# Kernel optimization log

Hardware: AMD Instinct MI355X
Metric: run time of the kernel (lower is better)

Reference implementation:

```python
import jax, jax.numpy as jnp
import numpy as np

N_NODES = 100000
D_SRC = 128
D_DST = 128
D_OUT = 256
N_EDGES = 600000


def setup_inputs() -> dict:
    key = jax.random.key(0)
    k1, k2, k3, k4, k5 = jax.random.split(key, 5)
    x_src = jax.random.normal(k1, (N_NODES, D_SRC), dtype=jnp.float32)
    x_dst = jax.random.normal(k2, (N_NODES, D_DST), dtype=jnp.float32)
    edge_index = jax.random.randint(k3, (2, N_EDGES), 0, N_NODES, dtype=jnp.int64)
    # Linear(in_src + in_dst, out): torch stores W as [out, in]
    fan_in = D_SRC + D_DST
    bound = 1.0 / np.sqrt(fan_in)
    W = jax.random.uniform(k4, (D_OUT, fan_in), minval=-bound, maxval=bound, dtype=jnp.float32)
    b = jax.random.uniform(k5, (D_OUT,), minval=-bound, maxval=bound, dtype=jnp.float32)
    return {"x_src": x_src, "x_dst": x_dst, "edge_index": edge_index, "W": W, "b": b}


def reference(x_src, x_dst, edge_index, W, b):
    src_idx, dst_idx = edge_index[0], edge_index[1]
    n_dst = x_dst.shape[0]
    x_j = x_src[src_idx]                                  # [E, D_SRC] gather
    summed = jax.ops.segment_sum(x_j, dst_idx, num_segments=n_dst)   # [N, D_SRC]
    count = jax.ops.segment_sum(jnp.ones((src_idx.shape[0],), dtype=x_src.dtype),
                                dst_idx, num_segments=n_dst)          # [N]
    agg = summed / jnp.maximum(count, 1.0)[:, None]        # scatter-mean
    h = jnp.concatenate([x_dst, agg], axis=-1)             # [N, D_DST+D_SRC]
    return jax.nn.relu(h @ W.T + b)                        # [N, D_OUT]
```

## Files before the change

kernel.cpp:

```cpp
#include <hip/hip_runtime.h>

#define N_NODES 100000
#define D_SRC 128
#define D_OUT 256
#define K_DIM 256
#define CAP 32
#define OVF_CAP 2048

typedef __attribute__((ext_vector_type(8))) short short8;
typedef __attribute__((ext_vector_type(4))) float float4v;

__device__ inline unsigned short f2bf(float f) {
    unsigned int u = __float_as_uint(f);
    u += 0x7FFF + ((u >> 16) & 1);
    return (unsigned short)(u >> 16);
}

__global__ __launch_bounds__(256) void bucket_kernel(
    const int* __restrict__ ei,
    int* __restrict__ deg,
    int* __restrict__ ovf_cnt,
    int* __restrict__ ovf,
    int* __restrict__ bucket,
    int n_edges)
{
    int e = blockIdx.x * 256 + threadIdx.x;
    if (e >= n_edges) return;
    int s = ei[e];
    int d = ei[n_edges + e];
    int pos = atomicAdd(deg + d, 1);
    if (pos < CAP) {
        bucket[(size_t)d * CAP + pos] = s;
    } else {
        int o = atomicAdd(ovf_cnt, 1);
        if (o < OVF_CAP) { ovf[2 * o] = s; ovf[2 * o + 1] = d; }
    }
}

__global__ __launch_bounds__(256) void gather_kernel(
    const float* __restrict__ x_src,
    const int*   __restrict__ deg,
    const int*   __restrict__ bucket,
    float*       __restrict__ agg)
{
    int node = blockIdx.x * 4 + (threadIdx.x >> 6);
    if (node >= N_NODES) return;
    int lane = threadIdx.x & 63;

    int n = deg[node];
    n = (n < CAP) ? n : CAP;

    int idx = bucket[(size_t)node * CAP + (lane & 31)];

    float2 acc0 = make_float2(0.f, 0.f);
    float2 acc1 = make_float2(0.f, 0.f);
    int i = 0;
    for (; i + 2 <= n; i += 2) {
        int s0 = __shfl(idx, i);
        int s1 = __shfl(idx, i + 1);
        float2 v0 = *(const float2*)(x_src + (size_t)s0 * D_SRC + lane * 2);
        float2 v1 = *(const float2*)(x_src + (size_t)s1 * D_SRC + lane * 2);
        acc0.x += v0.x; acc0.y += v0.y;
        acc1.x += v1.x; acc1.y += v1.y;
    }
    if (i < n) {
        int s0 = __shfl(idx, i);
        float2 v0 = *(const float2*)(x_src + (size_t)s0 * D_SRC + lane * 2);
        acc0.x += v0.x; acc0.y += v0.y;
    }
    acc0.x += acc1.x; acc0.y += acc1.y;
    *(float2*)(agg + (size_t)node * D_SRC + lane * 2) = acc0;
}

__global__ __launch_bounds__(256) void ovf_fixup_kernel(
    const float* __restrict__ x_src,
    const int* __restrict__ ovf_cnt,
    const int* __restrict__ ovf,
    float* __restrict__ agg)
{
    int e = blockIdx.x * 8 + (threadIdx.x >> 5);
    int lane = threadIdx.x & 31;
    int n = *ovf_cnt;
    if (n > OVF_CAP) n = OVF_CAP;
    if (e >= n) return;
    int s = ovf[2 * e];
    int d = ovf[2 * e + 1];
    float4 v = ((const float4*)(x_src + (size_t)s * D_SRC))[lane];
    float* a = agg + (size_t)d * D_SRC + lane * 4;
    unsafeAtomicAdd(a + 0, v.x);
    unsafeAtomicAdd(a + 1, v.y);
    unsafeAtomicAdd(a + 2, v.z);
    unsafeAtomicAdd(a + 3, v.w);
}

__global__ __launch_bounds__(256) void convert_w_kernel(
    const float* __restrict__ W, unsigned short* __restrict__ Wb)
{
    int i = blockIdx.x * 256 + threadIdx.x;
    float4 v = ((const float4*)W)[i];
    ushort4 o;
    o.x = f2bf(v.x); o.y = f2bf(v.y); o.z = f2bf(v.z); o.w = f2bf(v.w);
    ((ushort4*)Wb)[i] = o;
}

#define BM 128
#define BK 32
#define PADK 40

__global__ __launch_bounds__(512) void mfma_gemm_kernel(
    const float* __restrict__ x_dst,
    const float* __restrict__ agg,
    const int*   __restrict__ deg,
    const unsigned short* __restrict__ Wb,
    const float* __restrict__ bias,
    float*       __restrict__ out)
{
    __shared__ unsigned short As[BM * PADK];
    __shared__ unsigned short Bs[D_OUT * PADK];
    __shared__ float inv_s[BM];

    int t = threadIdx.x;
    int m0 = blockIdx.x * BM;

    if (t < BM) {
        int m = m0 + t;
        int c = (m < N_NODES) ? deg[m] : 1;
        inv_s[t] = 1.0f / (float)((c > 1) ? c : 1);
    }
    __syncthreads();

    int wave = t >> 6;
    int lane = t & 63;
    int wm = wave >> 2;
    int wn = wave & 3;
    int lrow = lane & 15;
    int kq = lane >> 4;

    float4v acc[4][4];
    #pragma unroll
    for (int i = 0; i < 4; ++i)
        #pragma unroll
        for (int j = 0; j < 4; ++j)
            acc[i][j] = (float4v){0.f, 0.f, 0.f, 0.f};

    int a_row  = t >> 2;
    int a_kseg = (t & 3) * 8;

    for (int kc = 0; kc < K_DIM / BK; ++kc) {
        int k0 = kc * BK;

        {
            bool is_agg = (k0 >= 128);
            const float* src = is_agg ? agg : x_dst;
            int koff = (is_agg ? k0 - 128 : k0) + a_kseg;
            int grow = m0 + a_row;
            float4 v0 = make_float4(0.f, 0.f, 0.f, 0.f);
            float4 v1 = v0;
            if (grow < N_NODES) {
                const float* p = src + (size_t)grow * D_SRC + koff;
                v0 = *(const float4*)p;
                v1 = *(const float4*)(p + 4);
            }
            if (is_agg) {
                float iv = inv_s[a_row];
                v0.x *= iv; v0.y *= iv; v0.z *= iv; v0.w *= iv;
                v1.x *= iv; v1.y *= iv; v1.z *= iv; v1.w *= iv;
            }
            union { unsigned short s[8]; short8 v; } pk;
            pk.s[0] = f2bf(v0.x); pk.s[1] = f2bf(v0.y);
            pk.s[2] = f2bf(v0.z); pk.s[3] = f2bf(v0.w);
            pk.s[4] = f2bf(v1.x); pk.s[5] = f2bf(v1.y);
            pk.s[6] = f2bf(v1.z); pk.s[7] = f2bf(v1.w);
            *(short8*)&As[a_row * PADK + a_kseg] = pk.v;
        }

        #pragma unroll
        for (int r = 0; r < 2; ++r) {
            int i = r * 512 + t;
            int row  = i >> 2;
            int kseg = (i & 3) * 8;
            short8 w = *(const short8*)(Wb + (size_t)row * K_DIM + k0 + kseg);
            *(short8*)&Bs[row * PADK + kseg] = w;
        }
        __syncthreads();

        short8 afrag[4], bfrag[4];
        #pragma unroll
        for (int mf = 0; mf < 4; ++mf)
            afrag[mf] = *(short8*)&As[(wm * 64 + mf * 16 + lrow) * PADK + kq * 8];
        #pragma unroll
        for (int nf = 0; nf < 4; ++nf)
            bfrag[nf] = *(short8*)&Bs[(wn * 64 + nf * 16 + lrow) * PADK + kq * 8];
        #pragma unroll
        for (int mf = 0; mf < 4; ++mf)
            #pragma unroll
            for (int nf = 0; nf < 4; ++nf)
                acc[mf][nf] = __builtin_amdgcn_mfma_f32_16x16x32_bf16(
                    afrag[mf], bfrag[nf], acc[mf][nf], 0, 0, 0);
        __syncthreads();
    }

    #pragma unroll
    for (int nf = 0; nf < 4; ++nf) {
        int col = wn * 64 + nf * 16 + lrow;
        float bv = bias[col];
        #pragma unroll
        for (int mf = 0; mf < 4; ++mf) {
            int rbase = m0 + wm * 64 + mf * 16 + kq * 4;
            #pragma unroll
            for (int r = 0; r < 4; ++r) {
                int row = rbase + r;
                if (row < N_NODES)
                    out[(size_t)row * D_OUT + col] = fmaxf(acc[mf][nf][r] + bv, 0.f);
            }
        }
    }
}

extern "C" void kernel_launch(void* const* d_in, const int* in_sizes, int n_in,
                              void* d_out, int out_size, void* d_ws, size_t ws_size,
                              hipStream_t stream) {
    const float* x_src = (const float*)d_in[0];
    const float* x_dst = (const float*)d_in[1];
    const int*   ei    = (const int*)d_in[2];
    const float* W     = (const float*)d_in[3];
    const float* bias  = (const float*)d_in[4];
    float* out = (float*)d_out;

    int n_edges = in_sizes[2] / 2;

    int* deg     = (int*)d_ws;
    int* ovf_cnt = deg + N_NODES;
    int* ovf     = ovf_cnt + 4;
    int* bucket  = ovf + OVF_CAP * 2;
    float* agg   = (float*)(bucket + (size_t)N_NODES * CAP);
    unsigned short* Wb = (unsigned short*)(agg + (size_t)N_NODES * D_SRC);

    hipMemsetAsync(d_ws, 0, (N_NODES + 4) * sizeof(int), stream);

    bucket_kernel<<<(n_edges + 255) / 256, 256, 0, stream>>>(
        ei, deg, ovf_cnt, ovf, bucket, n_edges);

    convert_w_kernel<<<(D_OUT * K_DIM / 4 + 255) / 256, 256, 0, stream>>>(W, Wb);

    gather_kernel<<<(N_NODES + 3) / 4, 256, 0, stream>>>(
        x_src, deg, bucket, agg);

    ovf_fixup_kernel<<<OVF_CAP / 8, 256, 0, stream>>>(
        x_src, ovf_cnt, ovf, agg);

    mfma_gemm_kernel<<<(N_NODES + BM - 1) / BM, 512, 0, stream>>>(
        x_dst, agg, deg, Wb, bias, out);
}
```

Before: 344.0 us.

## Fold overflow fixup and mean scaling into gather, store bf16 agg, drop LDS in GEMM

The gather kernel now handles overflow edges itself with a linear scan of the overflow list for high-degree nodes. It also applies the mean division and writes the aggregate as bf16, which halves agg traffic and removes the separate fixup launch. The GEMM drops shared-memory staging and barriers: each wave loads A and B fragments straight from global memory in MFMA layout, with 64-row blocks of 256 threads. The cost is redundant global reads of W and A across waves, which now rely on the cache. High-degree nodes also pay a serial scan of the overflow list.

```diff
diff --git a/kernel.cpp b/kernel.cpp
--- a/kernel.cpp
+++ b/kernel.cpp
@@ -41,14 +41,16 @@
     const float* __restrict__ x_src,
     const int*   __restrict__ deg,
     const int*   __restrict__ bucket,
-    float*       __restrict__ agg)
+    const int*   __restrict__ ovf_cnt,
+    const int*   __restrict__ ovf,
+    unsigned short* __restrict__ aggb)
 {
     int node = blockIdx.x * 4 + (threadIdx.x >> 6);
     if (node >= N_NODES) return;
     int lane = threadIdx.x & 63;
 
-    int n = deg[node];
-    n = (n < CAP) ? n : CAP;
+    int dtot = deg[node];
+    int n = (dtot < CAP) ? dtot : CAP;
 
     int idx = bucket[(size_t)node * CAP + (lane & 31)];
 
@@ -69,28 +71,23 @@
         acc0.x += v0.x; acc0.y += v0.y;
     }
     acc0.x += acc1.x; acc0.y += acc1.y;
-    *(float2*)(agg + (size_t)node * D_SRC + lane * 2) = acc0;
-}
-
-__global__ __launch_bounds__(256) void ovf_fixup_kernel(
-    const float* __restrict__ x_src,
-    const int* __restrict__ ovf_cnt,
-    const int* __restrict__ ovf,
-    float* __restrict__ agg)
-{
-    int e = blockIdx.x * 8 + (threadIdx.x >> 5);
-    int lane = threadIdx.x & 31;
-    int n = *ovf_cnt;
-    if (n > OVF_CAP) n = OVF_CAP;
-    if (e >= n) return;
-    int s = ovf[2 * e];
-    int d = ovf[2 * e + 1];
-    float4 v = ((const float4*)(x_src + (size_t)s * D_SRC))[lane];
-    float* a = agg + (size_t)d * D_SRC + lane * 4;
-    unsafeAtomicAdd(a + 0, v.x);
-    unsafeAtomicAdd(a + 1, v.y);
-    unsafeAtomicAdd(a + 2, v.z);
-    unsafeAtomicAdd(a + 3, v.w);
+
+    if (dtot > CAP) {
+        int oc = *ovf_cnt;
+        if (oc > OVF_CAP) oc = OVF_CAP;
+        for (int o = 0; o < oc; ++o) {
+            if (ovf[2 * o + 1] == node) {
+                int s0 = ovf[2 * o];
+                float2 v0 = *(const float2*)(x_src + (size_t)s0 * D_SRC + lane * 2);
+                acc0.x += v0.x; acc0.y += v0.y;
+            }
+        }
+    }
+
+    float inv = 1.0f / (float)((dtot > 1) ? dtot : 1);
+    unsigned int packed = (unsigned int)f2bf(acc0.x * inv)
+                        | ((unsigned int)f2bf(acc0.y * inv) << 16);
+    ((unsigned int*)(aggb + (size_t)node * D_SRC))[lane] = packed;
 }
 
 __global__ __launch_bounds__(256) void convert_w_kernel(
@@ -103,38 +100,19 @@
     ((ushort4*)Wb)[i] = o;
 }
 
-#define BM 128
-#define BK 32
-#define PADK 40
-
-__global__ __launch_bounds__(512) void mfma_gemm_kernel(
+__global__ __launch_bounds__(256) void mfma_gemm_kernel(
     const float* __restrict__ x_dst,
-    const float* __restrict__ agg,
-    const int*   __restrict__ deg,
+    const unsigned short* __restrict__ aggb,
     const unsigned short* __restrict__ Wb,
     const float* __restrict__ bias,
     float*       __restrict__ out)
 {
-    __shared__ unsigned short As[BM * PADK];
-    __shared__ unsigned short Bs[D_OUT * PADK];
-    __shared__ float inv_s[BM];
-
-    int t = threadIdx.x;
-    int m0 = blockIdx.x * BM;
-
-    if (t < BM) {
-        int m = m0 + t;
-        int c = (m < N_NODES) ? deg[m] : 1;
-        inv_s[t] = 1.0f / (float)((c > 1) ? c : 1);
-    }
-    __syncthreads();
-
-    int wave = t >> 6;
-    int lane = t & 63;
-    int wm = wave >> 2;
-    int wn = wave & 3;
+    int wave = threadIdx.x >> 6;
+    int lane = threadIdx.x & 63;
     int lrow = lane & 15;
-    int kq = lane >> 4;
+    int kq   = lane >> 4;
+    int m0 = blockIdx.x * 64;
+    int n0 = wave * 64;
 
     float4v acc[4][4];
     #pragma unroll
@@ -143,70 +121,65 @@
         for (int j = 0; j < 4; ++j)
             acc[i][j] = (float4v){0.f, 0.f, 0.f, 0.f};
 
-    int a_row  = t >> 2;
-    int a_kseg = (t & 3) * 8;
-
-    for (int kc = 0; kc < K_DIM / BK; ++kc) {
-        int k0 = kc * BK;
-
-        {
-            bool is_agg = (k0 >= 128);
-            const float* src = is_agg ? agg : x_dst;
-            int koff = (is_agg ? k0 - 128 : k0) + a_kseg;
-            int grow = m0 + a_row;
-            float4 v0 = make_float4(0.f, 0.f, 0.f, 0.f);
-            float4 v1 = v0;
-            if (grow < N_NODES) {
-                const float* p = src + (size_t)grow * D_SRC + koff;
-                v0 = *(const float4*)p;
-                v1 = *(const float4*)(p + 4);
+    int  rowv[4];
+    bool rok[4];
+    #pragma unroll
+    for (int mf = 0; mf < 4; ++mf) {
+        rowv[mf] = m0 + mf * 16 + lrow;
+        rok[mf]  = rowv[mf] < N_NODES;
+    }
+
+    const short8 zfrag = (short8){0,0,0,0,0,0,0,0};
+
+    #pragma unroll
+    for (int kc = 0; kc < 8; ++kc) {
+        const int k0 = kc * 32;
+        short8 afrag[4], bfrag[4];
+
+        if (kc < 4) {
+            #pragma unroll
+            for (int mf = 0; mf < 4; ++mf) {
+                float4 v0 = make_float4(0.f, 0.f, 0.f, 0.f);
+                float4 v1 = v0;
+                if (rok[mf]) {
+                    const float* p = x_dst + (size_t)rowv[mf] * D_SRC + k0 + kq * 8;
+                    v0 = *(const float4*)p;
+                    v1 = *(const float4*)(p + 4);
+                }
+                union { unsigned short s[8]; short8 v; } pk;
+                pk.s[0] = f2bf(v0.x); pk.s[1] = f2bf(v0.y);
+                pk.s[2] = f2bf(v0.z); pk.s[3] = f2bf(v0.w);
+                pk.s[4] = f2bf(v1.x); pk.s[5] = f2bf(v1.y);
+                pk.s[6] = f2bf(v1.z); pk.s[7] = f2bf(v1.w);
+                afrag[mf] = pk.v;
             }
-            if (is_agg) {
-                float iv = inv_s[a_row];
-                v0.x *= iv; v0.y *= iv; v0.z *= iv; v0.w *= iv;
-                v1.x *= iv; v1.y *= iv; v1.z *= iv; v1.w *= iv;
-            }
-            union { unsigned short s[8]; short8 v; } pk;
-            pk.s[0] = f2bf(v0.x); pk.s[1] = f2bf(v0.y);
-            pk.s[2] = f2bf(v0.z); pk.s[3] = f2bf(v0.w);
-            pk.s[4] = f2bf(v1.x); pk.s[5] = f2bf(v1.y);
-            pk.s[6] = f2bf(v1.z); pk.s[7] = f2bf(v1.w);
-            *(short8*)&As[a_row * PADK + a_kseg] = pk.v;
+        } else {
+            #pragma unroll
+            for (int mf = 0; mf < 4; ++mf)
+                afrag[mf] = rok[mf]
+                    ? *(const short8*)(aggb + (size_t)rowv[mf] * D_SRC + (k0 - 128) + kq * 8)
+                    : zfrag;
         }
 
         #pragma unroll
-        for (int r = 0; r < 2; ++r) {
-            int i = r * 512 + t;
-            int row  = i >> 2;
-            int kseg = (i & 3) * 8;
-            short8 w = *(const short8*)(Wb + (size_t)row * K_DIM + k0 + kseg);
-            *(short8*)&Bs[row * PADK + kseg] = w;
-        }
-        __syncthreads();
-
-        short8 afrag[4], bfrag[4];
-        #pragma unroll
-        for (int mf = 0; mf < 4; ++mf)
-            afrag[mf] = *(short8*)&As[(wm * 64 + mf * 16 + lrow) * PADK + kq * 8];
-        #pragma unroll
         for (int nf = 0; nf < 4; ++nf)
-            bfrag[nf] = *(short8*)&Bs[(wn * 64 + nf * 16 + lrow) * PADK + kq * 8];
+            bfrag[nf] = *(const short8*)(Wb + (size_t)(n0 + nf * 16 + lrow) * K_DIM + k0 + kq * 8);
+
         #pragma unroll
         for (int mf = 0; mf < 4; ++mf)
             #pragma unroll
             for (int nf = 0; nf < 4; ++nf)
                 acc[mf][nf] = __builtin_amdgcn_mfma_f32_16x16x32_bf16(
                     afrag[mf], bfrag[nf], acc[mf][nf], 0, 0, 0);
-        __syncthreads();
     }
 
     #pragma unroll
     for (int nf = 0; nf < 4; ++nf) {
-        int col = wn * 64 + nf * 16 + lrow;
+        int col = n0 + nf * 16 + lrow;
         float bv = bias[col];
         #pragma unroll
         for (int mf = 0; mf < 4; ++mf) {
-            int rbase = m0 + wm * 64 + mf * 16 + kq * 4;
+            int rbase = m0 + mf * 16 + kq * 4;
             #pragma unroll
             for (int r = 0; r < 4; ++r) {
                 int row = rbase + r;
@@ -233,8 +206,8 @@
     int* ovf_cnt = deg + N_NODES;
     int* ovf     = ovf_cnt + 4;
     int* bucket  = ovf + OVF_CAP * 2;
-    float* agg   = (float*)(bucket + (size_t)N_NODES * CAP);
-    unsigned short* Wb = (unsigned short*)(agg + (size_t)N_NODES * D_SRC);
+    unsigned short* aggb = (unsigned short*)(bucket + (size_t)N_NODES * CAP);
+    unsigned short* Wb   = aggb + (size_t)N_NODES * D_SRC;
 
     hipMemsetAsync(d_ws, 0, (N_NODES + 4) * sizeof(int), stream);
 
@@ -244,11 +217,8 @@
     convert_w_kernel<<<(D_OUT * K_DIM / 4 + 255) / 256, 256, 0, stream>>>(W, Wb);
 
     gather_kernel<<<(N_NODES + 3) / 4, 256, 0, stream>>>(
-        x_src, deg, bucket, agg);
-
-    ovf_fixup_kernel<<<OVF_CAP / 8, 256, 0, stream>>>(
-        x_src, ovf_cnt, ovf, agg);
-
-    mfma_gemm_kernel<<<(N_NODES + BM - 1) / BM, 512, 0, stream>>>(
-        x_dst, agg, deg, Wb, bias, out);
-}
+        x_src, deg, bucket, ovf_cnt, ovf, aggb);
+
+    mfma_gemm_kernel<<<(N_NODES + 63) / 64, 256, 0, stream>>>(
+        x_dst, aggb, Wb, bias, out);
+}
```

New measurement: 360.5 us. 4.8% more time.
